# Kernel optimization log

Hardware: AMD Instinct MI355X
Metric: run time of the kernel (lower is better)

## Reference

```python
import jax, jax.numpy as jnp
import numpy as np

B, L, CZ, CH = 1, 512, 128, 128
LN_EPS = 1e-5  # torch nn.LayerNorm default


def layer_norm(x, g, b, eps=LN_EPS):
    mu = jnp.mean(x, axis=-1, keepdims=True)
    var = jnp.var(x, axis=-1, keepdims=True)
    return (x - mu) * jax.lax.rsqrt(var + eps) * g + b


def setup_inputs() -> dict:
    key = jax.random.key(0)
    ks = jax.random.split(key, 16)
    def lin(k, fan_in, fan_out):
        bound = 1.0 / np.sqrt(fan_in)
        kw, kb = jax.random.split(k)
        W = jax.random.uniform(kw, (fan_out, fan_in), jnp.float32, -bound, bound)
        b = jax.random.uniform(kb, (fan_out,), jnp.float32, -bound, bound)
        return W, b
    z = jax.random.normal(ks[0], (B, L, L, CZ), jnp.float32)
    pair_mask = jnp.ones((B, L, L), jnp.float32)
    Wap, bap = lin(ks[1], CZ, CH)
    Wbp, bbp = lin(ks[2], CZ, CH)
    Wag, bag = lin(ks[3], CZ, CH)
    Wbg, bbg = lin(ks[4], CZ, CH)
    Wo, bo = lin(ks[5], CH, CZ)
    Wg, bg = lin(ks[6], CZ, CZ)
    return {
        "z": z, "pair_mask": pair_mask,
        "ln_in_g": jnp.ones((CZ,), jnp.float32), "ln_in_b": jnp.zeros((CZ,), jnp.float32),
        "Wap": Wap, "bap": bap, "Wbp": Wbp, "bbp": bbp,
        "Wag": Wag, "bag": bag, "Wbg": Wbg, "bbg": bbg,
        "ln_out_g": jnp.ones((CH,), jnp.float32), "ln_out_b": jnp.zeros((CH,), jnp.float32),
        "Wo": Wo, "bo": bo, "Wg": Wg, "bg": bg,
    }


def reference(z, pair_mask, ln_in_g, ln_in_b, Wap, bap, Wbp, bbp, Wag, bag,
              Wbg, bbg, ln_out_g, ln_out_b, Wo, bo, Wg, bg):
    # z: [B,L,L,c_z], pair_mask: [B,L,L]
    z_norm = layer_norm(z, ln_in_g, ln_in_b)
    a = (z_norm @ Wap.T + bap) * jax.nn.sigmoid(z_norm @ Wag.T + bag)  # [B,L,L,ch]
    b = (z_norm @ Wbp.T + bbp) * jax.nn.sigmoid(z_norm @ Wbg.T + bbg)
    m = pair_mask[..., None]
    a = a * m
    b = b * m
    # outgoing triangle contraction: c_hidden batched LxL matmuls
    x = jnp.einsum('bikc,bjkc->bijc', a, b)
    valid_k = jnp.einsum('bik,bjk->bij', pair_mask, pair_mask)
    x = x / jnp.sqrt(jnp.maximum(valid_k[..., None], 1.0))
    x = layer_norm(x, ln_out_g, ln_out_b)
    x = x @ Wo.T + bo
    gate = jax.nn.sigmoid(z_norm @ Wg.T + bg)
    x = x * gate  # dropout is identity in eval mode
    x = x * m
    return x
```

## Files before the change

### kernel.cpp

```cpp
#include <hip/hip_runtime.h>
#include <stdint.h>

typedef unsigned short u16;
typedef __bf16 bf16x8 __attribute__((ext_vector_type(8)));
typedef float  f32x4 __attribute__((ext_vector_type(4)));
typedef u16    u16x8 __attribute__((ext_vector_type(8)));
typedef u16    u16x4 __attribute__((ext_vector_type(4)));

constexpr int LL = 512;
constexpr int NROW = LL * LL;

__device__ __forceinline__ u16 f2b(float f) {
    __bf16 h = (__bf16)f;
    return __builtin_bit_cast(u16, h);
}
__device__ __forceinline__ float b2f(u16 s) {
    union { unsigned u; float f; } v; v.u = ((unsigned)s) << 16; return v.f;
}
__device__ __forceinline__ float sigmoidf_(float x) { return 1.0f / (1.0f + __expf(-x)); }

__device__ __forceinline__ f32x4 mfma16(bf16x8 a, bf16x8 b, f32x4 c) {
    return __builtin_amdgcn_mfma_f32_16x16x32_bf16(a, b, c, 0, 0, 0);
}

__global__ __launch_bounds__(256)
void k0_wconv(const float* __restrict__ Wap, const float* __restrict__ Wag,
              const float* __restrict__ Wbp, const float* __restrict__ Wbg,
              const float* __restrict__ Wg, const float* __restrict__ Wo,
              u16* __restrict__ wbf)
{
    const float* srcs[6] = {Wap, Wag, Wbp, Wbg, Wg, Wo};
    const int m = blockIdx.x >> 6;
    const int e = ((blockIdx.x & 63) << 8) | threadIdx.x;
    wbf[m * 16384 + e] = f2b(srcs[m][e]);
}

__global__ __launch_bounds__(256, 2)
void k1_ln_proj(const float* __restrict__ z, const float* __restrict__ mask,
                const float* __restrict__ lg, const float* __restrict__ lb,
                const u16* __restrict__ Wapb, const float* __restrict__ bap,
                const u16* __restrict__ Wagb, const float* __restrict__ bag,
                const u16* __restrict__ Wbpb, const float* __restrict__ bbp,
                const u16* __restrict__ Wbgb, const float* __restrict__ bbg,
                u16* __restrict__ a_t, u16* __restrict__ b_t,
                float* __restrict__ scale, float* zn_out)
{
    __shared__ __align__(16) u16 pool[18432];

    const int tid = threadIdx.x;
    const int lane = tid & 63, wave = tid >> 6;
    const int wm = (wave >> 1) * 64, wn = (wave & 1) * 64;
    const int lr = lane & 15, quad = lane >> 4, kq = quad * 8;

    if (blockIdx.x < 16) {
        u16 (*As)[72] = (u16(*)[72])pool;
        u16 (*Bs)[72] = (u16(*)[72])(pool + 128 * 72);
        const int sb = blockIdx.x;
        const int i0 = (sb >> 2) * 128, j0 = (sb & 3) * 128;

        f32x4 acc[4][4];
#pragma unroll
        for (int i = 0; i < 4; ++i)
#pragma unroll
            for (int j = 0; j < 4; ++j) acc[i][j] = (f32x4){0.f, 0.f, 0.f, 0.f};

        for (int kc = 0; kc < LL; kc += 64) {
#pragma unroll
            for (int p = 0; p < 8; ++p) {
                const int q = p * 256 + tid, rr = q >> 4, ko = (q & 15) * 4;
                f32x4 va = *(const f32x4*)(mask + (size_t)(i0 + rr) * LL + kc + ko);
                f32x4 vb = *(const f32x4*)(mask + (size_t)(j0 + rr) * LL + kc + ko);
                u16x4 ca, cb;
#pragma unroll
                for (int e = 0; e < 4; ++e) { ca[e] = f2b(va[e]); cb[e] = f2b(vb[e]); }
                *(u16x4*)&As[rr][ko] = ca;
                *(u16x4*)&Bs[rr][ko] = cb;
            }
            __syncthreads();
#pragma unroll
            for (int kk = 0; kk < 64; kk += 32) {
                bf16x8 af[4], bf[4];
#pragma unroll
                for (int mt = 0; mt < 4; ++mt) af[mt] = *(const bf16x8*)&As[wm + mt * 16 + lr][kk + kq];
#pragma unroll
                for (int nt = 0; nt < 4; ++nt) bf[nt] = *(const bf16x8*)&Bs[wn + nt * 16 + lr][kk + kq];
#pragma unroll
                for (int mt = 0; mt < 4; ++mt)
#pragma unroll
                    for (int nt = 0; nt < 4; ++nt) acc[mt][nt] = mfma16(af[mt], bf[nt], acc[mt][nt]);
            }
            __syncthreads();
        }
#pragma unroll
        for (int mt = 0; mt < 4; ++mt)
#pragma unroll
            for (int nt = 0; nt < 4; ++nt) {
                const int gj = j0 + wn + nt * 16 + lr;
#pragma unroll
                for (int e = 0; e < 4; ++e) {
                    const int gi = i0 + wm + mt * 16 + quad * 4 + e;
                    scale[(size_t)gi * LL + gj] = rsqrtf(fmaxf(acc[mt][nt][e], 1.0f));
                }
            }
        return;
    }

    u16 (*Zs)[136] = (u16(*)[136])pool;
    float* Gg = (float*)(pool + 17408);
    float* Gb = Gg + 128;
    float* Ms = Gb + 128;

    const int row0 = (blockIdx.x - 16) * 128;

    if (tid < 128) { Gg[tid] = lg[tid]; Gb[tid] = lb[tid]; Ms[tid] = mask[row0 + tid]; }

    {
        const int r = tid >> 1, h = (tid & 1) * 64;
        const float* zrow = z + (size_t)(row0 + r) * 128 + h;
        f32x4 zv[16];
        float s1 = 0.f, s2 = 0.f;
#pragma unroll
        for (int j = 0; j < 16; ++j) {
            zv[j] = *(const f32x4*)(zrow + j * 4);
#pragma unroll
            for (int e = 0; e < 4; ++e) { s1 += zv[j][e]; s2 += zv[j][e] * zv[j][e]; }
        }
        s1 += __shfl_xor(s1, 1);
        s2 += __shfl_xor(s2, 1);
        const float mu = s1 * 0.0078125f;
        const float rs = rsqrtf(fmaxf(s2 * 0.0078125f - mu * mu, 0.f) + 1e-5f);
        __syncthreads();
        u16* znb = (u16*)(zn_out + (size_t)row0 * 128) + r * 128 + h;
#pragma unroll
        for (int j = 0; j < 16; ++j) {
            u16x4 o;
#pragma unroll
            for (int e = 0; e < 4; ++e)
                o[e] = f2b((zv[j][e] - mu) * rs * Gg[h + j * 4 + e] + Gb[h + j * 4 + e]);
            *(u16x4*)&Zs[r][h + j * 4] = o;
            *(u16x4*)(znb + j * 4) = o;
        }
    }
    __syncthreads();

#pragma unroll 1
    for (int pair = 0; pair < 2; ++pair) {
        const u16* WP = pair ? Wbpb : Wapb;
        const float* BP = pair ? bbp : bap;
        const u16* WG = pair ? Wbgb : Wagb;
        const float* BG = pair ? bbg : bag;
        u16* outp = pair ? b_t : a_t;

        f32x4 accP[4][4], accG[4][4];
#pragma unroll
        for (int i = 0; i < 4; ++i)
#pragma unroll
            for (int j = 0; j < 4; ++j) {
                accP[i][j] = (f32x4){0.f, 0.f, 0.f, 0.f};
                accG[i][j] = (f32x4){0.f, 0.f, 0.f, 0.f};
            }
#pragma unroll
        for (int kk = 0; kk < 128; kk += 32) {
            bf16x8 af[4];
#pragma unroll
            for (int mt = 0; mt < 4; ++mt)
                af[mt] = *(const bf16x8*)&Zs[wm + mt * 16 + lr][kk + kq];
#pragma unroll
            for (int nt = 0; nt < 4; ++nt) {
                const int ncol = wn + nt * 16 + lr;
                bf16x8 bp8 = *(const bf16x8*)(WP + ncol * 128 + kk + kq);
                bf16x8 bg8 = *(const bf16x8*)(WG + ncol * 128 + kk + kq);
#pragma unroll
                for (int mt = 0; mt < 4; ++mt) {
                    accP[mt][nt] = mfma16(af[mt], bp8, accP[mt][nt]);
                    accG[mt][nt] = mfma16(af[mt], bg8, accG[mt][nt]);
                }
            }
        }
#pragma unroll
        for (int nt = 0; nt < 4; ++nt) {
            const int ncol = wn + nt * 16 + lr;
            const float bP = BP[ncol];
            const float bG = BG[ncol];
#pragma unroll
            for (int mt = 0; mt < 4; ++mt) {
                const int rb = wm + mt * 16 + quad * 4;
                u16x4 o;
#pragma unroll
                for (int e = 0; e < 4; ++e)
                    o[e] = f2b((accP[mt][nt][e] + bP) * sigmoidf_(accG[mt][nt][e] + bG) * Ms[rb + e]);
                *(u16x4*)(outp + (size_t)ncol * NROW + row0 + rb) = o;
            }
        }
    }
}

__global__ __launch_bounds__(256, 2)
void k3_einsum(const u16* __restrict__ a_t, const u16* __restrict__ b_t,
               const float* __restrict__ scale, u16* __restrict__ x_t)
{
    __shared__ __align__(16) u16 pool[2 * 128 * 136];
    u16 (*As)[136] = (u16(*)[136])pool;
    u16 (*Bs)[136] = (u16(*)[136])(pool + 128 * 136);
    u16 (*Ss)[128] = (u16(*)[128])pool;

    const int bid = blockIdx.x;
    const int xcd = bid & 7, slot = bid >> 3;
    const int c = xcd * 16 + (slot >> 4);
    const int tile = slot & 15;
    const int i0 = (tile >> 2) * 128, j0 = (tile & 3) * 128;

    const u16* A = a_t + (size_t)c * NROW;
    const u16* B = b_t + (size_t)c * NROW;

    const int tid = threadIdx.x;
    const int lane = tid & 63, wave = tid >> 6;
    const int wm = (wave >> 1) * 64, wn = (wave & 1) * 64;
    const int lr = lane & 15, quad = lane >> 4, kq = quad * 8;

    f32x4 acc[4][4];
#pragma unroll
    for (int i = 0; i < 4; ++i)
#pragma unroll
        for (int j = 0; j < 4; ++j) acc[i][j] = (f32x4){0.f, 0.f, 0.f, 0.f};

    for (int kc = 0; kc < LL; kc += 128) {
#pragma unroll
        for (int p = 0; p < 8; ++p) {
            const int q = p * 256 + tid, rr = q >> 4, ko = (q & 15) * 8;
            *(u16x8*)&As[rr][ko] = *(const u16x8*)(A + (size_t)(i0 + rr) * LL + kc + ko);
            *(u16x8*)&Bs[rr][ko] = *(const u16x8*)(B + (size_t)(j0 + rr) * LL + kc + ko);
        }
        __syncthreads();
#pragma unroll
        for (int kk = 0; kk < 128; kk += 32) {
            bf16x8 af[4], bf[4];
#pragma unroll
            for (int mt = 0; mt < 4; ++mt) af[mt] = *(const bf16x8*)&As[wm + mt * 16 + lr][kk + kq];
#pragma unroll
            for (int nt = 0; nt < 4; ++nt) bf[nt] = *(const bf16x8*)&Bs[wn + nt * 16 + lr][kk + kq];
#pragma unroll
            for (int mt = 0; mt < 4; ++mt)
#pragma unroll
                for (int nt = 0; nt < 4; ++nt) acc[mt][nt] = mfma16(af[mt], bf[nt], acc[mt][nt]);
        }
        __syncthreads();
    }
#pragma unroll
    for (int mt = 0; mt < 4; ++mt)
#pragma unroll
        for (int nt = 0; nt < 4; ++nt) {
            const int cc = wn + nt * 16 + lr;
#pragma unroll
            for (int e = 0; e < 4; ++e) {
                const int rr = wm + mt * 16 + quad * 4 + e;
                const float s = scale[(size_t)(i0 + rr) * LL + j0 + cc];
                Ss[rr][cc] = f2b(acc[mt][nt][e] * s);
            }
        }
    __syncthreads();
#pragma unroll
    for (int p = 0; p < 8; ++p) {
        const int rr = p * 16 + (tid >> 4);
        const int jo = (tid & 15) * 8;
        *(u16x8*)(x_t + (size_t)c * NROW + (size_t)(i0 + rr) * LL + j0 + jo) = *(const u16x8*)&Ss[rr][jo];
    }
}

__global__ __launch_bounds__(256, 2)
void k4_out(const u16* __restrict__ x_t, const float* __restrict__ mask,
            const float* __restrict__ lg, const float* __restrict__ lb,
            const u16* __restrict__ Wob, const float* __restrict__ bo,
            const u16* __restrict__ Wgb, const float* __restrict__ bgv,
            float* out)
{
    __shared__ __align__(16) u16 Zs[128][136];
    __shared__ __align__(16) u16 Zn[128][136];
    __shared__ float Ms[128];

    const int tid = threadIdx.x;
    const int row0 = blockIdx.x * 128;

    if (tid < 128) Ms[tid] = mask[row0 + tid];

    {
        const u16* znb = (const u16*)(out + (size_t)row0 * 128);
#pragma unroll
        for (int p = 0; p < 8; ++p) {
            const int idx = p * 256 + tid;
            const int rr = idx >> 4, co = (idx & 15) * 8;
            *(u16x8*)&Zn[rr][co] = *(const u16x8*)(znb + rr * 128 + co);
        }
    }

    {
        const int ijo = (tid & 31) * 4;
        const int cb = (tid >> 5) * 4;
#pragma unroll
        for (int p = 0; p < 4; ++p) {
            const int c = p * 32 + cb;
            u16x4 v0 = *(const u16x4*)(x_t + (size_t)(c + 0) * NROW + row0 + ijo);
            u16x4 v1 = *(const u16x4*)(x_t + (size_t)(c + 1) * NROW + row0 + ijo);
            u16x4 v2 = *(const u16x4*)(x_t + (size_t)(c + 2) * NROW + row0 + ijo);
            u16x4 v3 = *(const u16x4*)(x_t + (size_t)(c + 3) * NROW + row0 + ijo);
#pragma unroll
            for (int i = 0; i < 4; ++i) {
                u16x4 w = { v0[i], v1[i], v2[i], v3[i] };
                *(u16x4*)&Zs[ijo + i][c] = w;
            }
        }
    }
    __syncthreads();

    {
        const int r = tid >> 1, h = (tid & 1) * 64;
        float s1 = 0.f, s2 = 0.f;
#pragma unroll
        for (int j = 0; j < 64; j += 8) {
            u16x8 v = *(const u16x8*)&Zs[r][h + j];
#pragma unroll
            for (int e = 0; e < 8; ++e) { float x = b2f(v[e]); s1 += x; s2 += x * x; }
        }
        s1 += __shfl_xor(s1, 1);
        s2 += __shfl_xor(s2, 1);
        const float mu = s1 * 0.0078125f;
        const float rs = rsqrtf(fmaxf(s2 * 0.0078125f - mu * mu, 0.f) + 1e-5f);
#pragma unroll
        for (int j = 0; j < 64; j += 8) {
            const int c = h + j;
            u16x8 v = *(const u16x8*)&Zs[r][c];
            u16x8 o;
#pragma unroll
            for (int e = 0; e < 8; ++e)
                o[e] = f2b((b2f(v[e]) - mu) * rs * lg[c + e] + lb[c + e]);
            *(u16x8*)&Zs[r][c] = o;
        }
    }
    __syncthreads();

    const int lane = tid & 63, wave = tid >> 6;
    const int wm = (wave >> 1) * 64, wn = (wave & 1) * 64;
    const int lr = lane & 15, quad = lane >> 4, kq = quad * 8;

#pragma unroll 1
    for (int nh = 0; nh < 2; ++nh) {
        f32x4 accO[4][2], accG[4][2];
#pragma unroll
        for (int i = 0; i < 4; ++i)
#pragma unroll
            for (int j = 0; j < 2; ++j) {
                accO[i][j] = (f32x4){0.f, 0.f, 0.f, 0.f};
                accG[i][j] = (f32x4){0.f, 0.f, 0.f, 0.f};
            }
#pragma unroll
        for (int kk = 0; kk < 128; kk += 32) {
            bf16x8 ax[4], az[4];
#pragma unroll
            for (int mt = 0; mt < 4; ++mt) {
                ax[mt] = *(const bf16x8*)&Zs[wm + mt * 16 + lr][kk + kq];
                az[mt] = *(const bf16x8*)&Zn[wm + mt * 16 + lr][kk + kq];
            }
#pragma unroll
            for (int n2 = 0; n2 < 2; ++n2) {
                const int ncol = wn + (nh * 2 + n2) * 16 + lr;
                bf16x8 bo8 = *(const bf16x8*)(Wob + ncol * 128 + kk + kq);
                bf16x8 bg8 = *(const bf16x8*)(Wgb + ncol * 128 + kk + kq);
#pragma unroll
                for (int mt = 0; mt < 4; ++mt) {
                    accO[mt][n2] = mfma16(ax[mt], bo8, accO[mt][n2]);
                    accG[mt][n2] = mfma16(az[mt], bg8, accG[mt][n2]);
                }
            }
        }
#pragma unroll
        for (int n2 = 0; n2 < 2; ++n2) {
            const int cc = wn + (nh * 2 + n2) * 16 + lr;
            const float bb = bo[cc];
            const float bg = bgv[cc];
#pragma unroll
            for (int mt = 0; mt < 4; ++mt) {
                const int rb = wm + mt * 16 + quad * 4;
#pragma unroll
                for (int e = 0; e < 4; ++e) {
                    const size_t idx = (size_t)(row0 + rb + e) * 128 + cc;
                    out[idx] = (accO[mt][n2][e] + bb) * sigmoidf_(accG[mt][n2][e] + bg) * Ms[rb + e];
                }
            }
        }
    }
}

extern "C" void kernel_launch(void* const* d_in, const int* in_sizes, int n_in,
                              void* d_out, int out_size, void* d_ws, size_t ws_size,
                              hipStream_t stream)
{
    const float* z        = (const float*)d_in[0];
    const float* mask     = (const float*)d_in[1];
    const float* ln_in_g  = (const float*)d_in[2];
    const float* ln_in_b  = (const float*)d_in[3];
    const float* Wap      = (const float*)d_in[4];
    const float* bap      = (const float*)d_in[5];
    const float* Wbp      = (const float*)d_in[6];
    const float* bbp      = (const float*)d_in[7];
    const float* Wag      = (const float*)d_in[8];
    const float* bag      = (const float*)d_in[9];
    const float* Wbg      = (const float*)d_in[10];
    const float* bbg      = (const float*)d_in[11];
    const float* ln_out_g = (const float*)d_in[12];
    const float* ln_out_b = (const float*)d_in[13];
    const float* Wo       = (const float*)d_in[14];
    const float* bo       = (const float*)d_in[15];
    const float* Wg       = (const float*)d_in[16];
    const float* bg       = (const float*)d_in[17];

    u16* a_t = (u16*)d_ws;
    u16* b_t = a_t + (size_t)128 * NROW;
    u16* x_t = b_t + (size_t)128 * NROW;
    u16* wbf = x_t + (size_t)128 * NROW;
    float* scale = (float*)(wbf + 6 * 16384);
    float* outf  = (float*)d_out;

    const u16* Wapb = wbf + 0 * 16384;
    const u16* Wagb = wbf + 1 * 16384;
    const u16* Wbpb = wbf + 2 * 16384;
    const u16* Wbgb = wbf + 3 * 16384;
    const u16* Wgb  = wbf + 4 * 16384;
    const u16* Wob  = wbf + 5 * 16384;

    k0_wconv<<<dim3(384), dim3(256), 0, stream>>>(Wap, Wag, Wbp, Wbg, Wg, Wo, wbf);
    k1_ln_proj<<<dim3(2064), dim3(256), 0, stream>>>(z, mask, ln_in_g, ln_in_b,
        Wapb, bap, Wagb, bag, Wbpb, bbp, Wbgb, bbg, a_t, b_t, scale, outf);
    k3_einsum<<<dim3(2048), dim3(256), 0, stream>>>(a_t, b_t, scale, x_t);
    k4_out<<<dim3(2048), dim3(256), 0, stream>>>(x_t, mask, ln_out_g, ln_out_b,
        Wob, bo, Wgb, bg, outf);
}
```

Measured before the change: 614.8 us.

## Load einsum tiles with direct global-to-LDS loads and XOR-swizzled layout

Replaces the register-staged global-to-shared copies in the triangle einsum kernel with global_load_lds direct transfers of 16 bytes per lane. It halves the K chunk to 64, which shrinks shared memory from about 68KB to 32KB, and uses an XOR swizzle instead of row padding to avoid bank conflicts. The aim is to cut VGPR traffic and instruction count for loads and raise occupancy. In exchange it needs twice as many sync rounds per tile and stays single-buffered, with no overlap of load and compute.

New measurement: 599.9 us. 1.02x faster.

```diff
diff --git a/kernel.cpp b/kernel.cpp
--- a/kernel.cpp
+++ b/kernel.cpp
@@ -21,6 +21,12 @@
 
 __device__ __forceinline__ f32x4 mfma16(bf16x8 a, bf16x8 b, f32x4 c) {
     return __builtin_amdgcn_mfma_f32_16x16x32_bf16(a, b, c, 0, 0, 0);
+}
+
+__device__ __forceinline__ void glds16(const void* g, void* l) {
+    __builtin_amdgcn_global_load_lds(
+        (const __attribute__((address_space(1))) void*)g,
+        (__attribute__((address_space(3))) void*)l, 16, 0, 0);
 }
 
 __global__ __launch_bounds__(256)
@@ -199,9 +205,7 @@
 void k3_einsum(const u16* __restrict__ a_t, const u16* __restrict__ b_t,
                const float* __restrict__ scale, u16* __restrict__ x_t)
 {
-    __shared__ __align__(16) u16 pool[2 * 128 * 136];
-    u16 (*As)[136] = (u16(*)[136])pool;
-    u16 (*Bs)[136] = (u16(*)[136])(pool + 128 * 136);
+    __shared__ __align__(16) u16 pool[16384];
     u16 (*Ss)[128] = (u16(*)[128])pool;
 
     const int bid = blockIdx.x;
@@ -216,7 +220,13 @@
     const int tid = threadIdx.x;
     const int lane = tid & 63, wave = tid >> 6;
     const int wm = (wave >> 1) * 64, wn = (wave & 1) * 64;
-    const int lr = lane & 15, quad = lane >> 4, kq = quad * 8;
+    const int lr = lane & 15, quad = lane >> 4;
+
+    const int rsub = lane >> 3;
+    const int gsrc = (lane & 7) ^ rsub;
+    const char* Abase = (const char*)pool;
+    const char* Bbase = (const char*)pool + 16384;
+    const int sw0 = quad ^ (lr & 7);
 
     f32x4 acc[4][4];
 #pragma unroll
@@ -224,21 +234,29 @@
 #pragma unroll
         for (int j = 0; j < 4; ++j) acc[i][j] = (f32x4){0.f, 0.f, 0.f, 0.f};
 
-    for (int kc = 0; kc < LL; kc += 128) {
-#pragma unroll
-        for (int p = 0; p < 8; ++p) {
-            const int q = p * 256 + tid, rr = q >> 4, ko = (q & 15) * 8;
-            *(u16x8*)&As[rr][ko] = *(const u16x8*)(A + (size_t)(i0 + rr) * LL + kc + ko);
-            *(u16x8*)&Bs[rr][ko] = *(const u16x8*)(B + (size_t)(j0 + rr) * LL + kc + ko);
+    for (int kc = 0; kc < LL; kc += 64) {
+#pragma unroll
+        for (int i = 0; i < 4; ++i) {
+            const int chunk = wave * 4 + i;
+            const int r = chunk * 8 + rsub;
+            glds16(A + (size_t)(i0 + r) * LL + kc + gsrc * 8, pool + chunk * 512);
+            glds16(B + (size_t)(j0 + r) * LL + kc + gsrc * 8, pool + 8192 + chunk * 512);
         }
         __syncthreads();
 #pragma unroll
-        for (int kk = 0; kk < 128; kk += 32) {
+        for (int kk = 0; kk < 64; kk += 32) {
+            const int swg = sw0 ^ (kk >> 3);
             bf16x8 af[4], bf[4];
 #pragma unroll
-            for (int mt = 0; mt < 4; ++mt) af[mt] = *(const bf16x8*)&As[wm + mt * 16 + lr][kk + kq];
-#pragma unroll
-            for (int nt = 0; nt < 4; ++nt) bf[nt] = *(const bf16x8*)&Bs[wn + nt * 16 + lr][kk + kq];
+            for (int mt = 0; mt < 4; ++mt) {
+                const int R = wm + mt * 16 + lr;
+                af[mt] = *(const bf16x8*)(Abase + R * 128 + (swg << 4));
+            }
+#pragma unroll
+            for (int nt = 0; nt < 4; ++nt) {
+                const int R = wn + nt * 16 + lr;
+                bf[nt] = *(const bf16x8*)(Bbase + R * 128 + (swg << 4));
+            }
 #pragma unroll
             for (int mt = 0; mt < 4; ++mt)
 #pragma unroll
```
